# Kernel tuning notes

Measured on AMD Instinct MI355X. Metric: run time of the kernel, lower is better.

Reference implementation:

```python
import jax, jax.numpy as jnp
import numpy as np

IDIM = 128   # idim == odim (fc1 input dim must match shift-slice width idim_q)
HDIM = 1024
CDIM = 256
IGNORE_OUT = 10000.0


def setup_inputs() -> dict:
    key = jax.random.key(0)
    ks = jax.random.split(key, 4)
    B, T = 4, 512
    x = jax.random.normal(ks[0], (B, T, IDIM), dtype=jnp.float32)
    y = jax.random.normal(ks[1], (B, T, IDIM), dtype=jnp.float32)
    # xavier-ish init for the two linears (bias zeroed, as in initialize())
    w1 = jax.random.normal(ks[2], (HDIM, IDIM), dtype=jnp.float32) / np.sqrt(IDIM).astype(np.float32)
    b1 = jnp.zeros((HDIM,), jnp.float32)
    w2 = jax.random.normal(ks[3], (IDIM, HDIM), dtype=jnp.float32) / np.sqrt(HDIM).astype(np.float32)
    b2 = jnpts = jnp.zeros((IDIM,), jnp.float32)
    return {"x": x, "y": y, "w1": w1, "b1": b1, "w2": w2, "b2": b2}


def _shift_stack(key_seq, idim):
    """Vectorized _pad_for_shift: (B,T,idim) -> (B,T,2*idim-1,idim) shifted slices."""
    pad = idim - 1
    kp = jnp.pad(key_seq, ((0, 0), (0, 0), (pad, pad)))  # (B,T,3*idim-2)
    idx = jnp.arange(2 * idim - 1)[:, None] + jnp.arange(idim)[None, :]  # (S, idim)
    return kp[..., idx]  # (B,T,S,idim)


def _forward(x, y, w1, b1, w2, b2):
    idim = IDIM
    n_iter = HDIM // CDIM
    seq_mask = (y == IGNORE_OUT)                      # (B,T,odim)
    denom = jnp.sum(~seq_mask).astype(x.dtype)
    y_res, x_res = y, x
    losses = []
    for i in range(n_iter):
        # --- argaug (scale=False): sliding cosine cross-correlation + argmax ---
        kpt = _shift_stack(x_res, idim)               # (B,T,S,idim), S=2*idim-1
        num = jnp.einsum('btd,btsd->bts', y_res, kpt)
        den = jnp.linalg.norm(y_res, axis=-1)[..., None] * jnp.linalg.norm(kpt, axis=-1)
        sim = jnp.where(den == 0, 0.0, num / jnp.where(den == 0, 1.0, den))  # NaN(0/0) -> 0
        idx = jnp.argmax(sim, axis=-1)                # (B,T), first max like torch.max
        x_aug = jnp.take_along_axis(kpt, idx[..., None, None], axis=2)[..., 0, :]  # (B,T,idim)
        # --- attention (detached) ---
        attn = jax.lax.stop_gradient(jax.nn.softmax(x_aug * y_res, axis=-1))
        x_attn = x_aug * attn
        # --- _reverse_pad_for_shift: un-shift x_attn by 2*idim-2 - idx ---
        pad = idim - 1
        xap = jnp.pad(x_attn, ((0, 0), (0, 0), (pad, pad)))
        ridx = (2 * idim - 2 - idx)[..., None] + jnp.arange(idim)  # (B,T,idim)
        x_ele = jnp.take_along_axis(xap, ridx, axis=-1)
        # --- channel-masked two-layer MLP ---
        h = x_attn @ w1.T + b1                        # (B,T,hdim)
        m = jnp.zeros((HDIM,), x.dtype).at[i * CDIM:(i + 1) * CDIM].set(1.0)
        y_ele = (h * m) @ w2.T + b2                   # (B,T,odim)
        # --- masked MSE (sum of masked squared errors / #unmasked) ---
        sq = jnp.where(seq_mask, 0.0, (y_ele - y_res) ** 2)
        losses.append(jnp.sum(sq) / denom)
        y_res = y_res - y_ele
        x_res = x_res - x_ele
    return jnp.mean(jnp.stack(losses))


def reference(x, y, w1, b1, w2, b2):
    return _forward(x, y, w1, b1, w2, b2)
```

## Files before the change

### kernel.cpp

```cpp
#include <hip/hip_runtime.h>
#include <math.h>

#define NBLK  2048
#define NITER 4
#define IGNORE_OUT 10000.0f
#define LOG2E 1.44269504088896340736f

__device__ __forceinline__ float readlanef(float v, int lane){
  return __int_as_float(__builtin_amdgcn_readlane(__float_as_int(v), lane));
}

__device__ __forceinline__ float waveScanInc(float v){
  v += __int_as_float(__builtin_amdgcn_update_dpp(0, __float_as_int(v), 0x111, 0xF, 0xF, true));
  v += __int_as_float(__builtin_amdgcn_update_dpp(0, __float_as_int(v), 0x112, 0xF, 0xF, true));
  v += __int_as_float(__builtin_amdgcn_update_dpp(0, __float_as_int(v), 0x114, 0xF, 0xF, true));
  v += __int_as_float(__builtin_amdgcn_update_dpp(0, __float_as_int(v), 0x118, 0xF, 0xF, true));
  v += __int_as_float(__builtin_amdgcn_update_dpp(0, __float_as_int(v), 0x142, 0xA, 0xF, true));
  v += __int_as_float(__builtin_amdgcn_update_dpp(0, __float_as_int(v), 0x143, 0xC, 0xF, true));
  return v;
}
__device__ __forceinline__ float waveSum(float v){
  return readlanef(waveScanInc(v), 63);
}
__device__ __forceinline__ void waveArgmax(float &v, int &i){
#define AMSTEP(ctrl, rm) { \
    float ov = __int_as_float(__builtin_amdgcn_update_dpp(__float_as_int(v), __float_as_int(v), ctrl, rm, 0xF, false)); \
    int   oi = __builtin_amdgcn_update_dpp(i, i, ctrl, rm, 0xF, false); \
    bool take = (ov > v) || (ov == v && oi < i); \
    v = take ? ov : v; i = take ? oi : i; }
  AMSTEP(0x111, 0xF) AMSTEP(0x112, 0xF) AMSTEP(0x114, 0xF)
  AMSTEP(0x118, 0xF) AMSTEP(0x142, 0xA) AMSTEP(0x143, 0xC)
#undef AMSTEP
  v = readlanef(v, 63);
  i = __builtin_amdgcn_readlane(i, 63);
}
__device__ __forceinline__ void gatherPair(float v0, float v1, int idx, float &a, float &b){
  int c = idx & 63;
  float g0 = __shfl(v0, c, 64);
  float g1 = __shfl(v1, c, 64);
  a = ((unsigned)idx < 128u) ? ((idx & 64) ? g1 : g0) : 0.f;
  int idx2 = idx + 64;
  b = ((unsigned)idx2 < 128u) ? ((idx2 & 64) ? g1 : g0) : 0.f;
}

__global__ __launch_bounds__(512)
void prepK(const float* __restrict__ w1, const float* __restrict__ b1,
           const float* __restrict__ w2, const float* __restrict__ b2,
           float* __restrict__ M4, float* __restrict__ biasT, int* __restrict__ ticket){
  const int blk = blockIdx.x;
  const int tid = threadIdx.x;
  const int u = tid & 127, q = tid >> 7;
  __shared__ float part[512];
  if (blk < 512){
    int i = blk >> 7, o = blk & 127;
    const float* w1p = w1 + (i * 256 + q * 64) * 128 + u;
    const float* w2p = w2 + o * 1024 + i * 256 + q * 64;
    float a0 = 0.f, a1 = 0.f, a2 = 0.f, a3 = 0.f;
    #pragma unroll
    for (int c = 0; c < 64; c += 4){
      a0 = fmaf(w1p[(c + 0) * 128], w2p[c + 0], a0);
      a1 = fmaf(w1p[(c + 1) * 128], w2p[c + 1], a1);
      a2 = fmaf(w1p[(c + 2) * 128], w2p[c + 2], a2);
      a3 = fmaf(w1p[(c + 3) * 128], w2p[c + 3], a3);
    }
    part[tid] = (a0 + a1) + (a2 + a3);
    __syncthreads();
    if (q == 0)
      M4[i * 16384 + (u >> 2) * 512 + o * 4 + (u & 3)] =
          (part[u] + part[128 + u]) + (part[256 + u] + part[384 + u]);
  } else if (blk < 516){
    int i = blk - 512;
    const float* w2p = w2 + u * 1024 + i * 256 + q * 64;
    const float* b1p = b1 + i * 256 + q * 64;
    float a0 = (q == 0) ? b2[u] : 0.f, a1 = 0.f, a2 = 0.f, a3 = 0.f;
    #pragma unroll
    for (int c = 0; c < 64; c += 4){
      a0 = fmaf(b1p[c + 0], w2p[c + 0], a0);
      a1 = fmaf(b1p[c + 1], w2p[c + 1], a1);
      a2 = fmaf(b1p[c + 2], w2p[c + 2], a2);
      a3 = fmaf(b1p[c + 3], w2p[c + 3], a3);
    }
    part[tid] = (a0 + a1) + (a2 + a3);
    __syncthreads();
    if (q == 0)
      biasT[i * 128 + u] = (part[u] + part[128 + u]) + (part[256 + u] + part[384 + u]);
  } else {
    if (tid == 0) *ticket = 0;
  }
}

#define MLD(d0, d1, d2, d3, gg) \
  d0 = MpW[((gg) * 4 + 0) * 128]; d1 = MpW[((gg) * 4 + 1) * 128]; \
  d2 = MpW[((gg) * 4 + 2) * 128]; d3 = MpW[((gg) * 4 + 3) * 128];
#define MFM(m0, m1, m2, m3, src, kb) \
  a0 = fmaf((m0).x, readlanef(src, (kb) + 0), a0);  a0 = fmaf((m0).y, readlanef(src, (kb) + 1), a0); \
  a0 = fmaf((m0).z, readlanef(src, (kb) + 2), a0);  a0 = fmaf((m0).w, readlanef(src, (kb) + 3), a0); \
  a1 = fmaf((m1).x, readlanef(src, (kb) + 4), a1);  a1 = fmaf((m1).y, readlanef(src, (kb) + 5), a1); \
  a1 = fmaf((m1).z, readlanef(src, (kb) + 6), a1);  a1 = fmaf((m1).w, readlanef(src, (kb) + 7), a1); \
  a2 = fmaf((m2).x, readlanef(src, (kb) + 8), a2);  a2 = fmaf((m2).y, readlanef(src, (kb) + 9), a2); \
  a2 = fmaf((m2).z, readlanef(src, (kb) +10), a2);  a2 = fmaf((m2).w, readlanef(src, (kb) +11), a2); \
  a3 = fmaf((m3).x, readlanef(src, (kb) +12), a3);  a3 = fmaf((m3).y, readlanef(src, (kb) +13), a3); \
  a3 = fmaf((m3).z, readlanef(src, (kb) +14), a3);  a3 = fmaf((m3).w, readlanef(src, (kb) +15), a3);

__global__ __launch_bounds__(256, 4)
void mainK(const float* __restrict__ x, const float* __restrict__ y,
           const float* __restrict__ M4, const float* __restrict__ biasT,
           unsigned long long* __restrict__ partials, int* __restrict__ ticket,
           float* __restrict__ out){
  __shared__ float ydW[4][384];
  __shared__ float Ab[64], Bb[64], Cb[64], Db[64], Pb[64], Qb[64];
  __shared__ float mlpB[256];
  __shared__ float sL[4], sC[4];
  __shared__ int   sOld;

  const int u  = threadIdx.x;
  const int l  = u & 63;
  const int w  = u >> 6;
  const int th = w & 1;
  const int jh = w >> 1;
  const int o  = u & 127;
  const long base = (long)blockIdx.x * 128;

  float xlo = x[base + l], xhi = x[base + 64 + l];
  float ylo = y[base + l], yhi = y[base + 64 + l];
  const bool mask_l = (ylo == IGNORE_OUT);
  const bool mask_h = (yhi == IGNORE_OUT);
  float cnt = (w == 0) ? (mask_l ? 0.f : 1.f) : ((w == 1) ? (mask_h ? 0.f : 1.f) : 0.f);
  float lossAcc = 0.f;

  float* ydw = ydW[w];
  ydw[128 + l] = ylo; ydw[192 + l] = yhi; ydw[256 + l] = ylo; ydw[320 + l] = yhi;
  const float* wp = ydw + (255 - 64 * th + 64 * jh) - l;

  for (int i = 0; i < NITER; ++i){
    const float4* MpW = (const float4*)(M4 + (size_t)i * 16384) + jh * 2048 + o;
    float bias_l = biasT[i * 128 + l];
    float bias_h = biasT[i * 128 + 64 + l];

    const float xsrc = jh ? xhi : xlo;
    float s0=0.f,s1=0.f,s2=0.f,s3=0.f, p0=0.f,p1=0.f,p2=0.f,p3=0.f;
    if (w == 0 || w == 3){
      #pragma unroll
      for (int j = 0; j < 64; j += 4){
        float wv0 = wp[j], wv1 = wp[j+1], wv2 = wp[j+2], wv3 = wp[j+3];
        float x0 = readlanef(xsrc, j),   x1 = readlanef(xsrc, j+1);
        float x2 = readlanef(xsrc, j+2), x3 = readlanef(xsrc, j+3);
        s0 = fmaf(wv0, x0, s0); s1 = fmaf(wv1, x1, s1);
        s2 = fmaf(wv2, x2, s2); s3 = fmaf(wv3, x3, s3);
        p0 = fmaf((l >= j    ) ? wv0 : 0.f, x0, p0);
        p1 = fmaf((l >= j + 1) ? wv1 : 0.f, x1, p1);
        p2 = fmaf((l >= j + 2) ? wv2 : 0.f, x2, p2);
        p3 = fmaf((l >= j + 3) ? wv3 : 0.f, x3, p3);
      }
    } else {
      #pragma unroll
      for (int j = 0; j < 64; j += 4){
        float wv0 = wp[j], wv1 = wp[j+1], wv2 = wp[j+2], wv3 = wp[j+3];
        s0 = fmaf(wv0, readlanef(xsrc, j),   s0);
        s1 = fmaf(wv1, readlanef(xsrc, j+1), s1);
        s2 = fmaf(wv2, readlanef(xsrc, j+2), s2);
        s3 = fmaf(wv3, readlanef(xsrc, j+3), s3);
      }
    }
    float S = (s0 + s1) + (s2 + s3);
    float P = (p0 + p1) + (p2 + p3);
    if      (w == 0){ Ab[l] = S; Pb[l] = P; }
    else if (w == 1){ Bb[l] = S; }
    else if (w == 2){ Cb[l] = S; }
    else            { Db[l] = S; Qb[l] = P; }

    float v_lo = waveScanInc(xlo * xlo);
    float slo  = readlanef(v_lo, 63);
    float v_hi = waveScanInc(xhi * xhi);
    float shi  = readlanef(v_hi, 63);
    float total = slo + shi;
    float ny2 = waveSum(ylo * ylo + yhi * yhi);

    __syncthreads();

    float SA = Ab[l], SB = Bb[l], SC = Cb[l], SD = Db[l], PP = Pb[l], QQ = Qb[l];
    float nt_l = SA + SC, n1_l = PP;
    float nt_h = SB + SD, n1_h = SB + QQ;
    float pref_l = v_lo;
    float pref_h = v_hi + slo;
    int sstar;
    {
      bool yz = (ny2 == 0.f);
      float rNY = __builtin_amdgcn_rsqf(ny2);
      float nx_l = fmaxf(total - pref_l, 0.f);
      float nx_h = fmaxf(total - pref_h, 0.f);
      float s1l = (yz || pref_l == 0.f) ? 0.f : n1_l * __builtin_amdgcn_rsqf(pref_l) * rNY;
      float s2l = (yz || nx_l   == 0.f) ? 0.f : (nt_l - n1_l) * __builtin_amdgcn_rsqf(nx_l) * rNY;
      float s1h = (yz || pref_h == 0.f) ? 0.f : n1_h * __builtin_amdgcn_rsqf(pref_h) * rNY;
      float s2h = (yz || nx_h   == 0.f) ? 0.f : (nt_h - n1_h) * __builtin_amdgcn_rsqf(nx_h) * rNY;
      if (l == 63) s2h = -INFINITY;
      float bv = s1l; int bi = l;
      if (s1h > bv){ bv = s1h; bi = 64 + l; }
      if (s2l > bv){ bv = s2l; bi = 128 + l; }
      if (s2h > bv){ bv = s2h; bi = 192 + l; }
      waveArgmax(bv, bi);
      sstar = bi;
    }

    float4 A0, A1, A2, A3, B0, B1, B2, B3;
    MLD(A0, A1, A2, A3, 0)
    MLD(B0, B1, B2, B3, 1)

    float xa, xb;
    gatherPair(xlo, xhi, sstar + l - 127, xa, xb);
    float ea = __builtin_amdgcn_exp2f(xa * ylo * LOG2E);
    float eb = __builtin_amdgcn_exp2f(xb * yhi * LOG2E);
    float rse = __builtin_amdgcn_rcpf(waveSum(ea + eb));
    float wlo = xa * (ea * rse), whi = xb * (eb * rse);
    {
      float ga, gb;
      gatherPair(wlo, whi, l + 127 - sstar, ga, gb);
      xlo -= ga; xhi -= gb;
    }

    {
      const float wsrc = jh ? whi : wlo;
      float a0 = 0.f, a1 = 0.f, a2 = 0.f, a3 = 0.f;
      MFM(A0, A1, A2, A3, wsrc, 0)   MLD(A0, A1, A2, A3, 2)
      MFM(B0, B1, B2, B3, wsrc, 16)  MLD(B0, B1, B2, B3, 3)
      MFM(A0, A1, A2, A3, wsrc, 32)
      MFM(B0, B1, B2, B3, wsrc, 48)
      mlpB[u] = (a0 + a1) + (a2 + a3);
    }
    __syncthreads();

    {
      float ye_l = (mlpB[l]      + mlpB[128 + l]) + bias_l;
      float ye_h = (mlpB[64 + l] + mlpB[192 + l]) + bias_h;
      float df_l = ye_l - ylo, df_h = ye_h - yhi;
      if (w == 0 && !mask_l) lossAcc = fmaf(df_l, df_l, lossAcc);
      if (w == 1 && !mask_h) lossAcc = fmaf(df_h, df_h, lossAcc);
      ylo -= ye_l; yhi -= ye_h;
      ydw[128 + l] = ylo; ydw[192 + l] = yhi; ydw[256 + l] = ylo; ydw[320 + l] = yhi;
    }
  }

  lossAcc = waveSum(lossAcc);
  cnt     = waveSum(cnt);
  if (l == 0){ sL[w] = lossAcc; sC[w] = cnt; }
  __syncthreads();
  if (u == 0){
    union { float2 f; unsigned long long v; } pk;
    pk.f.x = (sL[0] + sL[1]) + (sL[2] + sL[3]);
    pk.f.y = (sC[0] + sC[1]) + (sC[2] + sC[3]);
    __hip_atomic_store(&partials[blockIdx.x], pk.v, __ATOMIC_RELEASE, __HIP_MEMORY_SCOPE_AGENT);
    sOld = __hip_atomic_fetch_add(ticket, 1, __ATOMIC_ACQ_REL, __HIP_MEMORY_SCOPE_AGENT);
  }
  __syncthreads();
  if (sOld == NBLK - 1){
    float ls = 0.f, cs = 0.f;
    for (int g = u; g < NBLK; g += 256){
      union { float2 f; unsigned long long v; } pk;
      pk.v = __hip_atomic_load(&partials[g], __ATOMIC_ACQUIRE, __HIP_MEMORY_SCOPE_AGENT);
      ls += pk.f.x; cs += pk.f.y;
    }
    ls = waveSum(ls); cs = waveSum(cs);
    if (l == 0){ sL[w] = ls; sC[w] = cs; }
    __syncthreads();
    if (u == 0) out[0] = ((sL[0] + sL[1]) + (sL[2] + sL[3])) /
                         ((float)NITER * ((sC[0] + sC[1]) + (sC[2] + sC[3])));
  }
}

extern "C" void kernel_launch(void* const* d_in, const int* in_sizes, int n_in,
                              void* d_out, int out_size, void* d_ws, size_t ws_size,
                              hipStream_t stream){
  const float* x  = (const float*)d_in[0];
  const float* y  = (const float*)d_in[1];
  const float* w1 = (const float*)d_in[2];
  const float* b1 = (const float*)d_in[3];
  const float* w2 = (const float*)d_in[4];
  const float* b2 = (const float*)d_in[5];
  float* out = (float*)d_out;

  int*   ticket = (int*)d_ws;
  float* M4     = (float*)((char*)d_ws + 256);
  float* biasT  = (float*)((char*)d_ws + 256 + 4 * 128 * 128 * sizeof(float));
  unsigned long long* partials =
      (unsigned long long*)((char*)d_ws + 256 + 4 * 128 * 128 * sizeof(float) + 4 * 128 * sizeof(float));

  prepK<<<517, 512, 0, stream>>>(w1, b1, w2, b2, M4, biasT, ticket);
  mainK<<<NBLK, 256, 0, stream>>>(x, y, M4, biasT, partials, ticket, out);
}
```

Measured before the change: 160.8 us.

## Process each row with a single wavefront instead of four cooperating waves

```diff
diff --git a/kernel.cpp b/kernel.cpp
--- a/kernel.cpp
+++ b/kernel.cpp
@@ -89,85 +89,50 @@
   }
 }
 
-#define MLD(d0, d1, d2, d3, gg) \
-  d0 = MpW[((gg) * 4 + 0) * 128]; d1 = MpW[((gg) * 4 + 1) * 128]; \
-  d2 = MpW[((gg) * 4 + 2) * 128]; d3 = MpW[((gg) * 4 + 3) * 128];
-#define MFM(m0, m1, m2, m3, src, kb) \
-  a0 = fmaf((m0).x, readlanef(src, (kb) + 0), a0);  a0 = fmaf((m0).y, readlanef(src, (kb) + 1), a0); \
-  a0 = fmaf((m0).z, readlanef(src, (kb) + 2), a0);  a0 = fmaf((m0).w, readlanef(src, (kb) + 3), a0); \
-  a1 = fmaf((m1).x, readlanef(src, (kb) + 4), a1);  a1 = fmaf((m1).y, readlanef(src, (kb) + 5), a1); \
-  a1 = fmaf((m1).z, readlanef(src, (kb) + 6), a1);  a1 = fmaf((m1).w, readlanef(src, (kb) + 7), a1); \
-  a2 = fmaf((m2).x, readlanef(src, (kb) + 8), a2);  a2 = fmaf((m2).y, readlanef(src, (kb) + 9), a2); \
-  a2 = fmaf((m2).z, readlanef(src, (kb) +10), a2);  a2 = fmaf((m2).w, readlanef(src, (kb) +11), a2); \
-  a3 = fmaf((m3).x, readlanef(src, (kb) +12), a3);  a3 = fmaf((m3).y, readlanef(src, (kb) +13), a3); \
-  a3 = fmaf((m3).z, readlanef(src, (kb) +14), a3);  a3 = fmaf((m3).w, readlanef(src, (kb) +15), a3);
-
-__global__ __launch_bounds__(256, 4)
+#define MLD2(pa,pb,pc,pd, qa,qb,qc,qd, gg) \
+  pa = MpL[((gg)*4+0)*128]; pb = MpL[((gg)*4+1)*128]; pc = MpL[((gg)*4+2)*128]; pd = MpL[((gg)*4+3)*128]; \
+  qa = MpH[((gg)*4+0)*128]; qb = MpH[((gg)*4+1)*128]; qc = MpH[((gg)*4+2)*128]; qd = MpH[((gg)*4+3)*128];
+#define MFM2(pa,pb,pc,pd, qa,qb,qc,qd, gg) { \
+  float4 xA = XW[4*(gg)+0], xB = XW[4*(gg)+1], xC = XW[4*(gg)+2], xD = XW[4*(gg)+3]; \
+  a0=fmaf((pa).x,xA.x,a0); a0=fmaf((pa).y,xA.y,a0); a0=fmaf((pa).z,xA.z,a0); a0=fmaf((pa).w,xA.w,a0); \
+  a1=fmaf((pb).x,xB.x,a1); a1=fmaf((pb).y,xB.y,a1); a1=fmaf((pb).z,xB.z,a1); a1=fmaf((pb).w,xB.w,a1); \
+  a2=fmaf((pc).x,xC.x,a2); a2=fmaf((pc).y,xC.y,a2); a2=fmaf((pc).z,xC.z,a2); a2=fmaf((pc).w,xC.w,a2); \
+  a3=fmaf((pd).x,xD.x,a3); a3=fmaf((pd).y,xD.y,a3); a3=fmaf((pd).z,xD.z,a3); a3=fmaf((pd).w,xD.w,a3); \
+  b0=fmaf((qa).x,xA.x,b0); b0=fmaf((qa).y,xA.y,b0); b0=fmaf((qa).z,xA.z,b0); b0=fmaf((qa).w,xA.w,b0); \
+  b1=fmaf((qb).x,xB.x,b1); b1=fmaf((qb).y,xB.y,b1); b1=fmaf((qb).z,xB.z,b1); b1=fmaf((qb).w,xB.w,b1); \
+  b2=fmaf((qc).x,xC.x,b2); b2=fmaf((qc).y,xC.y,b2); b2=fmaf((qc).z,xC.z,b2); b2=fmaf((qc).w,xC.w,b2); \
+  b3=fmaf((qd).x,xD.x,b3); b3=fmaf((qd).y,xD.y,b3); b3=fmaf((qd).z,xD.z,b3); b3=fmaf((qd).w,xD.w,b3); }
+
+__global__ __launch_bounds__(64, 2)
 void mainK(const float* __restrict__ x, const float* __restrict__ y,
            const float* __restrict__ M4, const float* __restrict__ biasT,
            unsigned long long* __restrict__ partials, int* __restrict__ ticket,
            float* __restrict__ out){
-  __shared__ float ydW[4][384];
-  __shared__ float Ab[64], Bb[64], Cb[64], Db[64], Pb[64], Qb[64];
-  __shared__ float mlpB[256];
-  __shared__ float sL[4], sC[4];
-  __shared__ int   sOld;
-
-  const int u  = threadIdx.x;
-  const int l  = u & 63;
-  const int w  = u >> 6;
-  const int th = w & 1;
-  const int jh = w >> 1;
-  const int o  = u & 127;
+  __shared__ float yd[384];
+  __shared__ float xsB[128];
+  __shared__ float xwB[128];
+
+  const int l = threadIdx.x;
   const long base = (long)blockIdx.x * 128;
 
   float xlo = x[base + l], xhi = x[base + 64 + l];
   float ylo = y[base + l], yhi = y[base + 64 + l];
   const bool mask_l = (ylo == IGNORE_OUT);
   const bool mask_h = (yhi == IGNORE_OUT);
-  float cnt = (w == 0) ? (mask_l ? 0.f : 1.f) : ((w == 1) ? (mask_h ? 0.f : 1.f) : 0.f);
-  float lossAcc = 0.f;
-
-  float* ydw = ydW[w];
-  ydw[128 + l] = ylo; ydw[192 + l] = yhi; ydw[256 + l] = ylo; ydw[320 + l] = yhi;
-  const float* wp = ydw + (255 - 64 * th + 64 * jh) - l;
+  float cntL = mask_l ? 0.f : 1.f, cntH = mask_h ? 0.f : 1.f;
+  float lossL = 0.f, lossH = 0.f;
+
+  yd[128 + l] = ylo; yd[192 + l] = yhi; yd[256 + l] = ylo; yd[320 + l] = yhi;
+  const float*  Wp = yd + (191 - l);
+  const float4* XS = (const float4*)xsB;
+  const float4* XW = (const float4*)xwB;
 
   for (int i = 0; i < NITER; ++i){
-    const float4* MpW = (const float4*)(M4 + (size_t)i * 16384) + jh * 2048 + o;
-    float bias_l = biasT[i * 128 + l];
-    float bias_h = biasT[i * 128 + 64 + l];
-
-    const float xsrc = jh ? xhi : xlo;
-    float s0=0.f,s1=0.f,s2=0.f,s3=0.f, p0=0.f,p1=0.f,p2=0.f,p3=0.f;
-    if (w == 0 || w == 3){
-      #pragma unroll
-      for (int j = 0; j < 64; j += 4){
-        float wv0 = wp[j], wv1 = wp[j+1], wv2 = wp[j+2], wv3 = wp[j+3];
-        float x0 = readlanef(xsrc, j),   x1 = readlanef(xsrc, j+1);
-        float x2 = readlanef(xsrc, j+2), x3 = readlanef(xsrc, j+3);
-        s0 = fmaf(wv0, x0, s0); s1 = fmaf(wv1, x1, s1);
-        s2 = fmaf(wv2, x2, s2); s3 = fmaf(wv3, x3, s3);
-        p0 = fmaf((l >= j    ) ? wv0 : 0.f, x0, p0);
-        p1 = fmaf((l >= j + 1) ? wv1 : 0.f, x1, p1);
-        p2 = fmaf((l >= j + 2) ? wv2 : 0.f, x2, p2);
-        p3 = fmaf((l >= j + 3) ? wv3 : 0.f, x3, p3);
-      }
-    } else {
-      #pragma unroll
-      for (int j = 0; j < 64; j += 4){
-        float wv0 = wp[j], wv1 = wp[j+1], wv2 = wp[j+2], wv3 = wp[j+3];
-        s0 = fmaf(wv0, readlanef(xsrc, j),   s0);
-        s1 = fmaf(wv1, readlanef(xsrc, j+1), s1);
-        s2 = fmaf(wv2, readlanef(xsrc, j+2), s2);
-        s3 = fmaf(wv3, readlanef(xsrc, j+3), s3);
-      }
-    }
-    float S = (s0 + s1) + (s2 + s3);
-    float P = (p0 + p1) + (p2 + p3);
-    if      (w == 0){ Ab[l] = S; Pb[l] = P; }
-    else if (w == 1){ Bb[l] = S; }
-    else if (w == 2){ Cb[l] = S; }
-    else            { Db[l] = S; Qb[l] = P; }
+    const float4* Mp  = (const float4*)(M4 + (size_t)i * 16384);
+    const float4* MpL = Mp + l;
+    const float4* MpH = Mp + 64 + l;
+
+    xsB[l] = xlo; xsB[64 + l] = xhi;
 
     float v_lo = waveScanInc(xlo * xlo);
     float slo  = readlanef(v_lo, 63);
@@ -176,13 +141,32 @@
     float total = slo + shi;
     float ny2 = waveSum(ylo * ylo + yhi * yhi);
 
-    __syncthreads();
-
-    float SA = Ab[l], SB = Bb[l], SC = Cb[l], SD = Db[l], PP = Pb[l], QQ = Qb[l];
-    float nt_l = SA + SC, n1_l = PP;
-    float nt_h = SB + SD, n1_h = SB + QQ;
+    float s0=0.f,s1=0.f,s2=0.f,s3=0.f, t0=0.f,t1=0.f,t2=0.f,t3=0.f, p0=0.f,p1=0.f,p2=0.f,p3=0.f;
+    float u0=0.f,u1=0.f,u2=0.f,u3=0.f, w0=0.f,w1=0.f,w2=0.f,w3=0.f, q0=0.f,q1=0.f,q2=0.f,q3=0.f;
+    #pragma unroll
+    for (int m = 0; m < 16; ++m){
+      float4 xvA = XS[m];
+      float4 xvB = XS[16 + m];
+      float g0a=Wp[4*m+0],  g0b=Wp[4*m+1],  g0c=Wp[4*m+2],  g0d=Wp[4*m+3];
+      float g1a=Wp[64+4*m], g1b=Wp[65+4*m], g1c=Wp[66+4*m], g1d=Wp[67+4*m];
+      float g2a=Wp[128+4*m],g2b=Wp[129+4*m],g2c=Wp[130+4*m],g2d=Wp[131+4*m];
+      const int jb = 4 * m;
+      u0=fmaf(g0a,xvA.x,u0); u1=fmaf(g0b,xvA.y,u1); u2=fmaf(g0c,xvA.z,u2); u3=fmaf(g0d,xvA.w,u3);
+      s0=fmaf(g1a,xvA.x,s0); s1=fmaf(g1b,xvA.y,s1); s2=fmaf(g1c,xvA.z,s2); s3=fmaf(g1d,xvA.w,s3);
+      p0=fmaf((l>=jb  )?g1a:0.f, xvA.x, p0); p1=fmaf((l>=jb+1)?g1b:0.f, xvA.y, p1);
+      p2=fmaf((l>=jb+2)?g1c:0.f, xvA.z, p2); p3=fmaf((l>=jb+3)?g1d:0.f, xvA.w, p3);
+      w0=fmaf(g1a,xvB.x,w0); w1=fmaf(g1b,xvB.y,w1); w2=fmaf(g1c,xvB.z,w2); w3=fmaf(g1d,xvB.w,w3);
+      q0=fmaf((l>=jb  )?g1a:0.f, xvB.x, q0); q1=fmaf((l>=jb+1)?g1b:0.f, xvB.y, q1);
+      q2=fmaf((l>=jb+2)?g1c:0.f, xvB.z, q2); q3=fmaf((l>=jb+3)?g1d:0.f, xvB.w, q3);
+      t0=fmaf(g2a,xvB.x,t0); t1=fmaf(g2b,xvB.y,t1); t2=fmaf(g2c,xvB.z,t2); t3=fmaf(g2d,xvB.w,t3);
+    }
+    float Sh0_l=(s0+s1)+(s2+s3), Sh1_l=(t0+t1)+(t2+t3), P=(p0+p1)+(p2+p3);
+    float Sh0_h=(u0+u1)+(u2+u3), Sh1_h=(w0+w1)+(w2+w3), Q=(q0+q1)+(q2+q3);
+    float nt_l = Sh0_l + Sh1_l, n1_l = P;
+    float nt_h = Sh0_h + Sh1_h, n1_h = Sh0_h + Q;
     float pref_l = v_lo;
     float pref_h = v_hi + slo;
+
     int sstar;
     {
       bool yz = (ny2 == 0.f);
@@ -202,9 +186,11 @@
       sstar = bi;
     }
 
-    float4 A0, A1, A2, A3, B0, B1, B2, B3;
-    MLD(A0, A1, A2, A3, 0)
-    MLD(B0, B1, B2, B3, 1)
+    float4 P0,P1,P2,P3, Q0,Q1,Q2,Q3, R0,R1,R2,R3, S0,S1,S2,S3;
+    MLD2(P0,P1,P2,P3, Q0,Q1,Q2,Q3, 0)
+    MLD2(R0,R1,R2,R3, S0,S1,S2,S3, 1)
+    float bias_l = biasT[i * 128 + l];
+    float bias_h = biasT[i * 128 + 64 + l];
 
     float xa, xb;
     gatherPair(xlo, xhi, sstar + l - 127, xa, xb);
@@ -212,58 +198,58 @@
     float eb = __builtin_amdgcn_exp2f(xb * yhi * LOG2E);
     float rse = __builtin_amdgcn_rcpf(waveSum(ea + eb));
     float wlo = xa * (ea * rse), whi = xb * (eb * rse);
+
     {
       float ga, gb;
       gatherPair(wlo, whi, l + 127 - sstar, ga, gb);
       xlo -= ga; xhi -= gb;
     }
 
-    {
-      const float wsrc = jh ? whi : wlo;
-      float a0 = 0.f, a1 = 0.f, a2 = 0.f, a3 = 0.f;
-      MFM(A0, A1, A2, A3, wsrc, 0)   MLD(A0, A1, A2, A3, 2)
-      MFM(B0, B1, B2, B3, wsrc, 16)  MLD(B0, B1, B2, B3, 3)
-      MFM(A0, A1, A2, A3, wsrc, 32)
-      MFM(B0, B1, B2, B3, wsrc, 48)
-      mlpB[u] = (a0 + a1) + (a2 + a3);
-    }
-    __syncthreads();
-
-    {
-      float ye_l = (mlpB[l]      + mlpB[128 + l]) + bias_l;
-      float ye_h = (mlpB[64 + l] + mlpB[192 + l]) + bias_h;
+    xwB[l] = wlo; xwB[64 + l] = whi;
+
+    float ye_l, ye_h;
+    {
+      float a0=0.f,a1=0.f,a2=0.f,a3=0.f, b0=0.f,b1=0.f,b2=0.f,b3=0.f;
+      MFM2(P0,P1,P2,P3, Q0,Q1,Q2,Q3, 0)  MLD2(P0,P1,P2,P3, Q0,Q1,Q2,Q3, 2)
+      MFM2(R0,R1,R2,R3, S0,S1,S2,S3, 1)  MLD2(R0,R1,R2,R3, S0,S1,S2,S3, 3)
+      MFM2(P0,P1,P2,P3, Q0,Q1,Q2,Q3, 2)  MLD2(P0,P1,P2,P3, Q0,Q1,Q2,Q3, 4)
+      MFM2(R0,R1,R2,R3, S0,S1,S2,S3, 3)  MLD2(R0,R1,R2,R3, S0,S1,S2,S3, 5)
+      MFM2(P0,P1,P2,P3, Q0,Q1,Q2,Q3, 4)  MLD2(P0,P1,P2,P3, Q0,Q1,Q2,Q3, 6)
+      MFM2(R0,R1,R2,R3, S0,S1,S2,S3, 5)  MLD2(R0,R1,R2,R3, S0,S1,S2,S3, 7)
+      MFM2(P0,P1,P2,P3, Q0,Q1,Q2,Q3, 6)
+      MFM2(R0,R1,R2,R3, S0,S1,S2,S3, 7)
+      ye_l = ((a0 + a1) + (a2 + a3)) + bias_l;
+      ye_h = ((b0 + b1) + (b2 + b3)) + bias_h;
+    }
+
+    {
       float df_l = ye_l - ylo, df_h = ye_h - yhi;
-      if (w == 0 && !mask_l) lossAcc = fmaf(df_l, df_l, lossAcc);
-      if (w == 1 && !mask_h) lossAcc = fmaf(df_h, df_h, lossAcc);
+      if (!mask_l) lossL = fmaf(df_l, df_l, lossL);
+      if (!mask_h) lossH = fmaf(df_h, df_h, lossH);
       ylo -= ye_l; yhi -= ye_h;
-      ydw[128 + l] = ylo; ydw[192 + l] = yhi; ydw[256 + l] = ylo; ydw[320 + l] = yhi;
-    }
-  }
-
-  lossAcc = waveSum(lossAcc);
-  cnt     = waveSum(cnt);
-  if (l == 0){ sL[w] = lossAcc; sC[w] = cnt; }
-  __syncthreads();
-  if (u == 0){
+      yd[128 + l] = ylo; yd[192 + l] = yhi; yd[256 + l] = ylo; yd[320 + l] = yhi;
+    }
+  }
+
+  float lsRow = waveSum(lossL) + waveSum(lossH);
+  float csRow = waveSum(cntL)  + waveSum(cntH);
+  int old = 0;
+  if (l == 0){
     union { float2 f; unsigned long long v; } pk;
-    pk.f.x = (sL[0] + sL[1]) + (sL[2] + sL[3]);
-    pk.f.y = (sC[0] + sC[1]) + (sC[2] + sC[3]);
+    pk.f.x = lsRow; pk.f.y = csRow;
     __hip_atomic_store(&partials[blockIdx.x], pk.v, __ATOMIC_RELEASE, __HIP_MEMORY_SCOPE_AGENT);
-    sOld = __hip_atomic_fetch_add(ticket, 1, __ATOMIC_ACQ_REL, __HIP_MEMORY_SCOPE_AGENT);
-  }
-  __syncthreads();
-  if (sOld == NBLK - 1){
+    old = __hip_atomic_fetch_add(ticket, 1, __ATOMIC_ACQ_REL, __HIP_MEMORY_SCOPE_AGENT);
+  }
+  old = __shfl(old, 0, 64);
+  if (old == NBLK - 1){
     float ls = 0.f, cs = 0.f;
-    for (int g = u; g < NBLK; g += 256){
+    for (int g = l; g < NBLK; g += 64){
       union { float2 f; unsigned long long v; } pk;
       pk.v = __hip_atomic_load(&partials[g], __ATOMIC_ACQUIRE, __HIP_MEMORY_SCOPE_AGENT);
       ls += pk.f.x; cs += pk.f.y;
     }
     ls = waveSum(ls); cs = waveSum(cs);
-    if (l == 0){ sL[w] = ls; sC[w] = cs; }
-    __syncthreads();
-    if (u == 0) out[0] = ((sL[0] + sL[1]) + (sL[2] + sL[3])) /
-                         ((float)NITER * ((sC[0] + sC[1]) + (sC[2] + sC[3])));
+    if (l == 0) out[0] = ls / ((float)NITER * cs);
   }
 }
 
@@ -285,5 +271,5 @@
       (unsigned long long*)((char*)d_ws + 256 + 4 * 128 * 128 * sizeof(float) + 4 * 128 * sizeof(float));
 
   prepK<<<517, 512, 0, stream>>>(w1, b1, w2, b2, M4, biasT, ticket);
-  mainK<<<NBLK, 256, 0, stream>>>(x, y, M4, biasT, partials, ticket, out);
-}
+  mainK<<<NBLK, 64, 0, stream>>>(x, y, M4, biasT, partials, ticket, out);
+}
```

After: 155.4 us. -3.3%, faster.
